# Kernel tuning notes

Measured on AMD Instinct MI355X. Metric: run time of the kernel, lower is better.

The kernel has to match this reference:

```python
import jax, jax.numpy as jnp
import numpy as np
import itertools

# --- constants matching init_kwargs / chosen problem size ---
MOD = 6.283185307179586       # 2*pi, modular wrap for angular error
DEG_U = 90.0                  # deg_u
DEG_P = 1.0                   # deg_p (grid resolution in degrees)
D = 4                         # number of active sources (ones per label row)
NUM_CLASSES = 181             # angle grid size
BATCH = 131072

# All D! permutations as one-hot matrices: exact LAP solution by brute force
# (equivalent to lap.lapjv on the square DxD cost matrix).
_PERMS = np.array(list(itertools.permutations(range(D))), dtype=np.int32)   # (D!, D)
PERM_OH = jnp.asarray(np.eye(D, dtype=np.float32)[_PERMS])                  # (D!, D, D)


def setup_inputs() -> dict:
    key = jax.random.key(0)
    k1, k2 = jax.random.split(key)
    # predicted DOAs live in the first D slots of logits (radians)
    logits = jax.random.normal(k1, (BATCH, NUM_CLASSES), dtype=jnp.float32)
    # labels: exactly D ones per row (D distinct grid indices)
    scores = jax.random.uniform(k2, (BATCH, NUM_CLASSES))
    idx = jnp.argsort(scores, axis=1)[:, :D]                     # D distinct cols per row
    labels = jnp.zeros((BATCH, NUM_CLASSES), dtype=jnp.int32)
    labels = labels.at[jnp.arange(BATCH)[:, None], idx].set(1)
    return {"logits": logits, "labels": labels}


def _sq_mod_diff(a, b):
    # ((a - b + mod/2) % mod - mod/2)**2 : squared wrapped angular error
    d = jnp.mod(a - b + MOD / 2, MOD) - MOD / 2
    return d * d


def reference(logits, labels):
    # np.where(labels==1)[0] returns ascending indices of the ones.
    # Stable ascending argsort of a 0/1 row puts the one-indices (in ascending
    # order) in the last D slots.
    one_idx = jnp.argsort(labels, axis=1)[:, -D:]                        # (B, D)
    label_ang = (one_idx.astype(jnp.float32) * DEG_P - DEG_U) * (jnp.pi / 180.0)  # (B, D) radians

    doa = logits[:, :D]                                                  # (B, D)
    # per-sample DxD cost matrix of squared modular errors
    cost = _sq_mod_diff(doa[:, :, None], label_ang[:, None, :])          # (B, D, D)
    # optimal assignment = min total cost over all permutations (exact LAP)
    totals = jnp.einsum('bij,pij->bp', cost, PERM_OH)                    # (B, D!)
    min_total = jnp.min(totals, axis=1)                                  # (B,)
    rmse = jnp.sqrt(min_total / D)                                       # (B,)
    return rmse.mean()
```

## Files before the change

kernel.cpp:

```cpp
#include <hip/hip_runtime.h>
#include <hip/hip_bf16.h>
#include <math.h>

constexpr int   NC      = 181;
constexpr int   BATCH   = 131072;
constexpr float MODC    = 6.2831853071795864769f;
constexpr float HALFMOD = 3.1415926535897932385f;
constexpr float DEG2RAD = 0.017453292519943295f;

constexpr unsigned MAGIC181 = 23729102u;

constexpr int K1 = 8;

__device__ __forceinline__ void deposit(unsigned g, unsigned* __restrict__ bm) {
    const unsigned row = __umulhi(g, MAGIC181);
    const unsigned cls = g - 181u * row;
    atomicOr(&bm[row * 8u + (cls >> 5)], 1u << (cls & 31u));
}

__global__ __launch_bounds__(256) void scan_kernel(
    const int*    __restrict__ labels,
    unsigned*     __restrict__ bm)
{
    const size_t base = (size_t)blockIdx.x * (256 * K1) + threadIdx.x;
    const int4* p4 = (const int4*)labels;

    int4 v[K1];
    #pragma unroll
    for (int j = 0; j < K1; ++j)
        v[j] = p4[base + (size_t)j * 256];

    #pragma unroll
    for (int j = 0; j < K1; ++j) {
        const unsigned g0 = (unsigned)(base + (size_t)j * 256) * 4u;
        if (v[j].x != 0) deposit(g0 + 0u, bm);
        if (v[j].y != 0) deposit(g0 + 1u, bm);
        if (v[j].z != 0) deposit(g0 + 2u, bm);
        if (v[j].w != 0) deposit(g0 + 3u, bm);
    }
}

__device__ __forceinline__ float sq_mod_diff(float x) {
    float t = x + HALFMOD;
    float m = t - floorf(t * (1.0f / MODC)) * MODC;
    float d = m - HALFMOD;
    return d * d;
}

__global__ __launch_bounds__(256) void finish_kernel(
    const float*    __restrict__ logits,
    const unsigned* __restrict__ bm,
    float*          __restrict__ out)
{
    const int row = blockIdx.x * 256 + threadIdx.x;

    const uint4 w0 = ((const uint4*)bm)[(size_t)row * 2 + 0];
    const uint4 w1 = ((const uint4*)bm)[(size_t)row * 2 + 1];
    const float* lp = logits + (size_t)row * NC;
    const float doa[4] = {lp[0], lp[1], lp[2], lp[3]};

    unsigned w[8] = {w0.x, w0.y, w0.z, w0.w, w1.x, w1.y, w1.z, w1.w};
    float ang[4];
    int found = 0;
    #pragma unroll
    for (int k = 0; k < 8; ++k) {
        unsigned mm = w[k];
        while (mm) {
            const int j = __builtin_ctz(mm);
            mm &= mm - 1;
            ang[found & 3] = ((float)(k * 32 + j) - 90.0f) * DEG2RAD;
            ++found;
        }
    }

    float cst[4][4];
    #pragma unroll
    for (int i = 0; i < 4; ++i)
        #pragma unroll
        for (int j = 0; j < 4; ++j)
            cst[i][j] = sq_mod_diff(doa[i] - ang[j]);

    float best = 1e30f;
    #pragma unroll
    for (int a = 0; a < 4; ++a) {
        #pragma unroll
        for (int b = 0; b < 4; ++b) {
            if (b == a) continue;
            const float top = cst[0][a] + cst[1][b];
            #pragma unroll
            for (int e = 0; e < 4; ++e) {
                if (e == a || e == b) continue;
                const int f = 6 - a - b - e;
                best = fminf(best, top + cst[2][e] + cst[3][f]);
            }
        }
    }
    float sum = sqrtf(best * 0.25f);

    #pragma unroll
    for (int off = 32; off > 0; off >>= 1)
        sum += __shfl_down(sum, off);

    __shared__ float wsum[4];
    const int lane = threadIdx.x & 63;
    const int wv   = threadIdx.x >> 6;
    if (lane == 0) wsum[wv] = sum;
    __syncthreads();
    if (threadIdx.x == 0) {
        float t = (wsum[0] + wsum[1]) + (wsum[2] + wsum[3]);
        atomicAdd(out, t * (1.0f / (float)BATCH));
    }
}

extern "C" void kernel_launch(void* const* d_in, const int* in_sizes, int n_in,
                              void* d_out, int out_size, void* d_ws, size_t ws_size,
                              hipStream_t stream) {
    const float* logits = (const float*)d_in[0];
    const int*   labels = (const int*)d_in[1];
    float*       out    = (float*)d_out;

    unsigned* bm = (unsigned*)d_ws;

    hipMemsetAsync(out, 0, sizeof(float), stream);
    hipMemsetAsync(bm, 0, (size_t)BATCH * 32, stream);

    scan_kernel<<<2896, 256, 0, stream>>>(labels, bm);
    finish_kernel<<<BATCH / 256, 256, 0, stream>>>(logits, bm, out);
}
```

Measured before the change: 198.0 us.

## Fuse label scan and assignment into one kernel with shared-memory bitmap

```diff
diff --git a/kernel.cpp b/kernel.cpp
--- a/kernel.cpp
+++ b/kernel.cpp
@@ -10,35 +10,10 @@
 
 constexpr unsigned MAGIC181 = 23729102u;
 
-constexpr int K1 = 8;
-
-__device__ __forceinline__ void deposit(unsigned g, unsigned* __restrict__ bm) {
-    const unsigned row = __umulhi(g, MAGIC181);
-    const unsigned cls = g - 181u * row;
-    atomicOr(&bm[row * 8u + (cls >> 5)], 1u << (cls & 31u));
-}
-
-__global__ __launch_bounds__(256) void scan_kernel(
-    const int*    __restrict__ labels,
-    unsigned*     __restrict__ bm)
-{
-    const size_t base = (size_t)blockIdx.x * (256 * K1) + threadIdx.x;
-    const int4* p4 = (const int4*)labels;
-
-    int4 v[K1];
-    #pragma unroll
-    for (int j = 0; j < K1; ++j)
-        v[j] = p4[base + (size_t)j * 256];
-
-    #pragma unroll
-    for (int j = 0; j < K1; ++j) {
-        const unsigned g0 = (unsigned)(base + (size_t)j * 256) * 4u;
-        if (v[j].x != 0) deposit(g0 + 0u, bm);
-        if (v[j].y != 0) deposit(g0 + 1u, bm);
-        if (v[j].z != 0) deposit(g0 + 2u, bm);
-        if (v[j].w != 0) deposit(g0 + 3u, bm);
-    }
-}
+constexpr int RPB   = 256;
+constexpr int WINT4 = RPB * NC / 4;
+constexpr int NPT   = WINT4 / 1024;
+constexpr int REM   = WINT4 - NPT * 1024;
 
 __device__ __forceinline__ float sq_mod_diff(float x) {
     float t = x + HALFMOD;
@@ -47,67 +22,110 @@
     return d * d;
 }
 
-__global__ __launch_bounds__(256) void finish_kernel(
-    const float*    __restrict__ logits,
-    const unsigned* __restrict__ bm,
-    float*          __restrict__ out)
+__device__ __forceinline__ void deposit(unsigned g, unsigned rowBase,
+                                        unsigned* __restrict__ bm) {
+    const unsigned row  = __umulhi(g, MAGIC181);
+    const unsigned cls  = g - 181u * row;
+    const unsigned lrow = row - rowBase;
+    atomicOr(&bm[lrow * 8u + (cls >> 5u)], 1u << (cls & 31u));
+}
+
+__global__ __launch_bounds__(1024) void fused_kernel(
+    const float* __restrict__ logits,
+    const int*   __restrict__ labels,
+    float*       __restrict__ out)
 {
-    const int row = blockIdx.x * 256 + threadIdx.x;
+    __shared__ unsigned bm[RPB * 8];
+    __shared__ float    wsum[4];
 
-    const uint4 w0 = ((const uint4*)bm)[(size_t)row * 2 + 0];
-    const uint4 w1 = ((const uint4*)bm)[(size_t)row * 2 + 1];
-    const float* lp = logits + (size_t)row * NC;
-    const float doa[4] = {lp[0], lp[1], lp[2], lp[3]};
+    const int tid = threadIdx.x;
+    const unsigned rowBase = blockIdx.x * RPB;
 
-    unsigned w[8] = {w0.x, w0.y, w0.z, w0.w, w1.x, w1.y, w1.z, w1.w};
-    float ang[4];
-    int found = 0;
+    bm[tid]        = 0u;
+    bm[tid + 1024] = 0u;
+    __syncthreads();
+
+    const unsigned base4 = (unsigned)blockIdx.x * WINT4 + tid;
+    const int4* p4 = (const int4*)labels;
+    int4 v[NPT + 1];
     #pragma unroll
-    for (int k = 0; k < 8; ++k) {
-        unsigned mm = w[k];
-        while (mm) {
-            const int j = __builtin_ctz(mm);
-            mm &= mm - 1;
-            ang[found & 3] = ((float)(k * 32 + j) - 90.0f) * DEG2RAD;
-            ++found;
+    for (int k = 0; k < NPT; ++k)
+        v[k] = p4[(size_t)base4 + (size_t)k * 1024];
+    {
+        int4 t = {0, 0, 0, 0};
+        if (tid < REM) t = p4[(size_t)base4 + (size_t)NPT * 1024];
+        v[NPT] = t;
+    }
+
+    float d0 = 0.f, d1 = 0.f, d2 = 0.f, d3 = 0.f;
+    if (tid < RPB) {
+        const float* lp = logits + (size_t)(rowBase + tid) * NC;
+        d0 = lp[0]; d1 = lp[1]; d2 = lp[2]; d3 = lp[3];
+    }
+
+    #pragma unroll
+    for (int k = 0; k < NPT + 1; ++k) {
+        const int4 w = v[k];
+        if ((w.x | w.y | w.z | w.w) != 0) {
+            const unsigned g0 = (base4 + (unsigned)k * 1024u) * 4u;
+            if (w.x != 0) deposit(g0 + 0u, rowBase, bm);
+            if (w.y != 0) deposit(g0 + 1u, rowBase, bm);
+            if (w.z != 0) deposit(g0 + 2u, rowBase, bm);
+            if (w.w != 0) deposit(g0 + 3u, rowBase, bm);
         }
     }
+    __syncthreads();
 
-    float cst[4][4];
-    #pragma unroll
-    for (int i = 0; i < 4; ++i)
+    float sum = 0.0f;
+    if (tid < RPB) {
+        const float doa[4] = {d0, d1, d2, d3};
+
+        float ang[4];
+        int found = 0;
         #pragma unroll
-        for (int j = 0; j < 4; ++j)
-            cst[i][j] = sq_mod_diff(doa[i] - ang[j]);
-
-    float best = 1e30f;
-    #pragma unroll
-    for (int a = 0; a < 4; ++a) {
-        #pragma unroll
-        for (int b = 0; b < 4; ++b) {
-            if (b == a) continue;
-            const float top = cst[0][a] + cst[1][b];
-            #pragma unroll
-            for (int e = 0; e < 4; ++e) {
-                if (e == a || e == b) continue;
-                const int f = 6 - a - b - e;
-                best = fminf(best, top + cst[2][e] + cst[3][f]);
+        for (int k = 0; k < 8; ++k) {
+            unsigned mm = bm[tid * 8 + k];
+            while (mm) {
+                const int j = __builtin_ctz(mm);
+                mm &= mm - 1;
+                ang[found & 3] = ((float)(k * 32 + j) - 90.0f) * DEG2RAD;
+                ++found;
             }
         }
+
+        float cst[4][4];
+        #pragma unroll
+        for (int i = 0; i < 4; ++i)
+            #pragma unroll
+            for (int j = 0; j < 4; ++j)
+                cst[i][j] = sq_mod_diff(doa[i] - ang[j]);
+
+        float best = 1e30f;
+        #pragma unroll
+        for (int a = 0; a < 4; ++a) {
+            #pragma unroll
+            for (int b = 0; b < 4; ++b) {
+                if (b == a) continue;
+                const float top = cst[0][a] + cst[1][b];
+                #pragma unroll
+                for (int e = 0; e < 4; ++e) {
+                    if (e == a || e == b) continue;
+                    const int f = 6 - a - b - e;
+                    best = fminf(best, top + cst[2][e] + cst[3][f]);
+                }
+            }
+        }
+        sum = sqrtf(best * 0.25f);
+
+        #pragma unroll
+        for (int off = 32; off > 0; off >>= 1)
+            sum += __shfl_down(sum, off);
+        if ((tid & 63) == 0) wsum[tid >> 6] = sum;
     }
-    float sum = sqrtf(best * 0.25f);
+    __syncthreads();
 
-    #pragma unroll
-    for (int off = 32; off > 0; off >>= 1)
-        sum += __shfl_down(sum, off);
-
-    __shared__ float wsum[4];
-    const int lane = threadIdx.x & 63;
-    const int wv   = threadIdx.x >> 6;
-    if (lane == 0) wsum[wv] = sum;
-    __syncthreads();
-    if (threadIdx.x == 0) {
-        float t = (wsum[0] + wsum[1]) + (wsum[2] + wsum[3]);
+    if (tid == 0) {
+        const float t = (wsum[0] + wsum[1]) + (wsum[2] + wsum[3]);
         atomicAdd(out, t * (1.0f / (float)BATCH));
     }
 }
@@ -119,11 +137,7 @@
     const int*   labels = (const int*)d_in[1];
     float*       out    = (float*)d_out;
 
-    unsigned* bm = (unsigned*)d_ws;
+    hipMemsetAsync(out, 0, sizeof(float), stream);
 
-    hipMemsetAsync(out, 0, sizeof(float), stream);
-    hipMemsetAsync(bm, 0, (size_t)BATCH * 32, stream);
-
-    scan_kernel<<<2896, 256, 0, stream>>>(labels, bm);
-    finish_kernel<<<BATCH / 256, 256, 0, stream>>>(logits, bm, out);
+    fused_kernel<<<BATCH / RPB, 1024, 0, stream>>>(logits, labels, out);
 }
```

Measured after the change: 194.1 us. 1.02x faster.

## Split label scan into branchless bitmask pass and sparse decode pass

Applied to the files above, without the earlier changes.

```diff
diff --git a/kernel.cpp b/kernel.cpp
--- a/kernel.cpp
+++ b/kernel.cpp
@@ -10,33 +10,62 @@
 
 constexpr unsigned MAGIC181 = 23729102u;
 
-constexpr int K1 = 8;
+constexpr int TOT4  = BATCH * NC / 4;
+constexpr int NMASK = TOT4 / 8;
 
-__device__ __forceinline__ void deposit(unsigned g, unsigned* __restrict__ bm) {
-    const unsigned row = __umulhi(g, MAGIC181);
-    const unsigned cls = g - 181u * row;
-    atomicOr(&bm[row * 8u + (cls >> 5)], 1u << (cls & 31u));
+__global__ __launch_bounds__(256) void mask_kernel(
+    const int*  __restrict__ labels,
+    unsigned*   __restrict__ masks)
+{
+    const int tid = threadIdx.x;
+    const unsigned base4 = blockIdx.x * 2048u + (unsigned)tid;
+    const int4* p4 = (const int4*)labels;
+
+    int4 v[8];
+    #pragma unroll
+    for (int k = 0; k < 8; ++k)
+        v[k] = p4[base4 + 256u * k];
+
+    __builtin_amdgcn_sched_barrier(0);
+
+    unsigned m = 0u;
+    #pragma unroll
+    for (int k = 0; k < 8; ++k) {
+        m |= ((unsigned)(v[k].x != 0)) << (4 * k + 0);
+        m |= ((unsigned)(v[k].y != 0)) << (4 * k + 1);
+        m |= ((unsigned)(v[k].z != 0)) << (4 * k + 2);
+        m |= ((unsigned)(v[k].w != 0)) << (4 * k + 3);
+    }
+    masks[blockIdx.x * 256u + (unsigned)tid] = m;
 }
 
-__global__ __launch_bounds__(256) void scan_kernel(
-    const int*    __restrict__ labels,
-    unsigned*     __restrict__ bm)
+__global__ __launch_bounds__(256) void decode_kernel(
+    const unsigned* __restrict__ masks,
+    unsigned*       __restrict__ bm)
 {
-    const size_t base = (size_t)blockIdx.x * (256 * K1) + threadIdx.x;
-    const int4* p4 = (const int4*)labels;
+    const unsigned base = blockIdx.x * 1024u + (unsigned)threadIdx.x;
 
-    int4 v[K1];
+    unsigned mw[4];
     #pragma unroll
-    for (int j = 0; j < K1; ++j)
-        v[j] = p4[base + (size_t)j * 256];
+    for (int j = 0; j < 4; ++j)
+        mw[j] = masks[base + 256u * j];
+
+    __builtin_amdgcn_sched_barrier(0);
 
     #pragma unroll
-    for (int j = 0; j < K1; ++j) {
-        const unsigned g0 = (unsigned)(base + (size_t)j * 256) * 4u;
-        if (v[j].x != 0) deposit(g0 + 0u, bm);
-        if (v[j].y != 0) deposit(g0 + 1u, bm);
-        if (v[j].z != 0) deposit(g0 + 2u, bm);
-        if (v[j].w != 0) deposit(g0 + 3u, bm);
+    for (int j = 0; j < 4; ++j) {
+        const unsigned d = base + 256u * j;
+        unsigned w = mw[j];
+        while (w) {
+            const int b = __builtin_ctz(w);
+            w &= w - 1;
+            const unsigned i4 = ((d >> 8) << 11) + (d & 255u)
+                              + (((unsigned)b >> 2) << 8);
+            const unsigned g   = i4 * 4u + ((unsigned)b & 3u);
+            const unsigned row = __umulhi(g, MAGIC181);
+            const unsigned cls = g - 181u * row;
+            atomicOr(&bm[row * 8u + (cls >> 5u)], 1u << (cls & 31u));
+        }
     }
 }
 
@@ -119,11 +148,13 @@
     const int*   labels = (const int*)d_in[1];
     float*       out    = (float*)d_out;
 
-    unsigned* bm = (unsigned*)d_ws;
+    unsigned* bm    = (unsigned*)d_ws;
+    unsigned* masks = (unsigned*)((char*)d_ws + (size_t)BATCH * 32);
 
     hipMemsetAsync(out, 0, sizeof(float), stream);
     hipMemsetAsync(bm, 0, (size_t)BATCH * 32, stream);
 
-    scan_kernel<<<2896, 256, 0, stream>>>(labels, bm);
-    finish_kernel<<<BATCH / 256, 256, 0, stream>>>(logits, bm, out);
+    mask_kernel  <<<2896,          256, 0, stream>>>(labels, masks);
+    decode_kernel<<<NMASK / 1024,  256, 0, stream>>>(masks, bm);
+    finish_kernel<<<BATCH / 256,   256, 0, stream>>>(logits, bm, out);
 }
```

New measurement: 208.3 us. 1.05x slower.
